# Performance work log

Measured on AMD Instinct MI355X. Metric: run time of the kernel, lower is better.

## Reference

```python
import jax, jax.numpy as jnp
import numpy as np

N = 50000      # nodes
E = 800000     # directed edges (before self-loops)
IN = 128       # input feature dim
HID = 64       # per-head hidden channels (concat=False -> head mean)
H = 4          # attention heads
OUT = 1
NEG_SLOPE = 0.2


def setup_inputs() -> dict:
    key = jax.random.key(0)
    ks = jax.random.split(key, 20)
    def glorot(k, shape, fan):
        return jax.random.normal(k, shape, jnp.float32) * (1.0 / np.sqrt(fan))
    inp = {
        "x": jax.random.normal(ks[0], (N, IN), jnp.float32),
        "edge_index": jax.random.randint(ks[1], (2, E), 0, N, jnp.int32),
        # layer 1
        "W1": glorot(ks[2], (IN, H * HID), IN),
        "a_s1": glorot(ks[3], (H, HID), HID),
        "a_d1": glorot(ks[4], (H, HID), HID),
        "b1": jnp.zeros((HID,), jnp.float32),
        # layer 2
        "W2": glorot(ks[5], (HID, H * HID), HID),
        "a_s2": glorot(ks[6], (H, HID), HID),
        "a_d2": glorot(ks[7], (H, HID), HID),
        "b2": jnp.zeros((HID,), jnp.float32),
        # layer 3
        "W3": glorot(ks[8], (HID, H * HID), HID),
        "a_s3": glorot(ks[9], (H, HID), HID),
        "a_d3": glorot(ks[10], (H, HID), HID),
        "b3": jnp.zeros((HID,), jnp.float32),
        # final linear
        "fc_W": glorot(ks[11], (HID, OUT), HID),
        "fc_b": jnp.zeros((OUT,), jnp.float32),
    }
    return inp


def _gat_layer(x, src, dst, W, a_s, a_d, b):
    """PyG GATConv with concat=False (mean over heads), self-loops already in src/dst."""
    n = x.shape[0]
    h = (x @ W).reshape(n, H, -1)                      # [N,H,C]
    es = jnp.einsum('nhc,hc->nh', h, a_s)              # [N,H] alpha_src per node
    ed = jnp.einsum('nhc,hc->nh', h, a_d)              # [N,H] alpha_dst per node
    e = jax.nn.leaky_relu(es[src] + ed[dst], NEG_SLOPE)  # [E,H] per-edge logits
    # segment softmax over edges sharing the same dst (every node has a self-loop)
    m = jax.ops.segment_max(e, dst, num_segments=n)
    w = jnp.exp(e - m[dst])
    z = jax.ops.segment_sum(w, dst, num_segments=n)
    alpha = w / z[dst]                                  # [E,H]
    out = jax.ops.segment_sum(alpha[:, :, None] * h[src], dst, num_segments=n)  # [N,H,C]
    return out.mean(axis=1) + b                         # concat=False -> head mean + bias


def reference(x, edge_index, W1, a_s1, a_d1, b1, W2, a_s2, a_d2, b2,
              W3, a_s3, a_d3, b3, fc_W, fc_b):
    n = x.shape[0]
    loops = jnp.arange(n, dtype=edge_index.dtype)
    src = jnp.concatenate([edge_index[0], loops])
    dst = jnp.concatenate([edge_index[1], loops])
    gelu = lambda t: jax.nn.gelu(t, approximate=False)  # torch F.gelu default = exact erf
    x = gelu(_gat_layer(x, src, dst, W1, a_s1, a_d1, b1))
    x = gelu(_gat_layer(x, src, dst, W2, a_s2, a_d2, b2))
    x = gelu(_gat_layer(x, src, dst, W3, a_s3, a_d3, b3))
    # dropout is identity in eval mode (deterministic reference)
    return jax.nn.sigmoid(x @ fc_W + fc_b)              # [N,1]
```

## Files before the change

kernel.cpp:

```cpp
#include <hip/hip_runtime.h>
#include <math.h>

#define N_NODES 50000
#define N_EDGES 800000
#define ETOT    (N_EDGES + N_NODES)
#define DIM_IN  128
#define HID     64
#define NHEAD   4
#define HDIM    256
#define NEG_SLOPE 0.2f

typedef __attribute__((ext_vector_type(8))) short bf16x8;
typedef __attribute__((ext_vector_type(4))) float f32x4;

static __device__ __forceinline__ float gelu_exact(float x) {
    return 0.5f * x * (1.0f + erff(x * 0.70710678118654752f));
}
static __device__ __forceinline__ unsigned short f2bf(float f) {
    unsigned u = __float_as_uint(f);
    u = (u + 0x7FFFu + ((u >> 16) & 1u)) >> 16;
    return (unsigned short)u;
}

__global__ void count_conv_kernel(const int* __restrict__ ei, int* __restrict__ counts,
                                  int* __restrict__ eslot,
                                  const float* __restrict__ W1, const float* __restrict__ W2,
                                  const float* __restrict__ W3,
                                  unsigned short* __restrict__ Wt1, unsigned short* __restrict__ Wt2,
                                  unsigned short* __restrict__ Wt3) {
    int i = blockIdx.x * 256 + threadIdx.x;
    if (i < 65536) {
        if (i < 32768) {
            int k = i >> 8, n = i & 255;
            Wt1[n * DIM_IN + k] = f2bf(W1[i]);
        } else if (i < 49152) {
            int l = i - 32768; int k = l >> 8, n = l & 255;
            Wt2[n * HID + k] = f2bf(W2[l]);
        } else {
            int l = i - 49152; int k = l >> 8, n = l & 255;
            Wt3[n * HID + k] = f2bf(W3[l]);
        }
    }
    if (i >= ETOT) return;
    int d = (i < N_EDGES) ? ei[N_EDGES + i] : (i - N_EDGES);
    eslot[i] = atomicAdd(&counts[d], 1);
}

__global__ void scan1_kernel(const int* __restrict__ counts, int* __restrict__ offs,
                             int* __restrict__ blockSums) {
    __shared__ int s[256];
    int t = threadIdx.x, idx = blockIdx.x * 256 + t;
    int v = (idx < N_NODES) ? counts[idx] : 0;
    s[t] = v; __syncthreads();
    #pragma unroll
    for (int o = 1; o < 256; o <<= 1) {
        int add = (t >= o) ? s[t - o] : 0;
        __syncthreads();
        s[t] += add;
        __syncthreads();
    }
    if (idx < N_NODES) offs[idx] = s[t] - v;
    if (t == 255) blockSums[blockIdx.x] = s[t];
}

__global__ void scan2_kernel(const int* __restrict__ blockSums, int* __restrict__ blockScan, int nb) {
    __shared__ int s[256];
    int t = threadIdx.x;
    int v = (t < nb) ? blockSums[t] : 0;
    s[t] = v; __syncthreads();
    #pragma unroll
    for (int o = 1; o < 256; o <<= 1) {
        int add = (t >= o) ? s[t - o] : 0;
        __syncthreads();
        s[t] += add;
        __syncthreads();
    }
    blockScan[t] = s[t] - v;
}

__global__ void scan3_kernel(int* __restrict__ offs, const int* __restrict__ blockScan) {
    int idx = blockIdx.x * 256 + threadIdx.x;
    if (idx < N_NODES) offs[idx] += blockScan[blockIdx.x];
    if (idx == 0) offs[N_NODES] = ETOT;
}

__global__ void fill_kernel(const int* __restrict__ ei, const int* __restrict__ offs,
                            const int* __restrict__ eslot, int* __restrict__ coff) {
    int i = blockIdx.x * 256 + threadIdx.x;
    if (i >= ETOT) return;
    int s, d;
    if (i < N_EDGES) { s = ei[i]; d = ei[N_EDGES + i]; } else { s = d = i - N_EDGES; }
    coff[offs[d] + eslot[i]] = s << 9;
}

template<int K, bool F32A>
__global__ __launch_bounds__(256) void gemm_mfma_kernel(
    const void* __restrict__ Aptr, const unsigned short* __restrict__ Wt,
    const float* __restrict__ a_s, const float* __restrict__ a_d,
    unsigned short* __restrict__ h_bf, float* __restrict__ es, float* __restrict__ ed,
    int M)
{
    constexpr int KS = K / 32;
    __shared__ unsigned short hstage[64][HDIM + 8];
    const int lane = threadIdx.x & 63;
    const int head = threadIdx.x >> 6;
    const int l15 = lane & 15;
    const int lg  = lane >> 4;
    const int row0 = blockIdx.x * 64;

    bf16x8 bfrag[4][KS];
    #pragma unroll
    for (int n = 0; n < 4; ++n)
        #pragma unroll
        for (int ks = 0; ks < KS; ++ks)
            bfrag[n][ks] = *(const bf16x8*)(Wt + (size_t)(head * 64 + n * 16 + l15) * K + ks * 32 + lg * 8);

    f32x4 acc[4][4];
    #pragma unroll
    for (int m = 0; m < 4; ++m)
        #pragma unroll
        for (int n = 0; n < 4; ++n)
            acc[m][n] = (f32x4){0.f, 0.f, 0.f, 0.f};

    #pragma unroll
    for (int m = 0; m < 4; ++m) {
        int row = row0 + m * 16 + l15;
        if (row >= M) row = M - 1;
        #pragma unroll
        for (int ks = 0; ks < KS; ++ks) {
            bf16x8 af;
            if constexpr (F32A) {
                const float* ap = (const float*)Aptr + (size_t)row * K + ks * 32 + lg * 8;
                float4 u0 = *(const float4*)(ap);
                float4 u1 = *(const float4*)(ap + 4);
                af[0] = (short)f2bf(u0.x); af[1] = (short)f2bf(u0.y);
                af[2] = (short)f2bf(u0.z); af[3] = (short)f2bf(u0.w);
                af[4] = (short)f2bf(u1.x); af[5] = (short)f2bf(u1.y);
                af[6] = (short)f2bf(u1.z); af[7] = (short)f2bf(u1.w);
            } else {
                af = *(const bf16x8*)((const unsigned short*)Aptr + (size_t)row * K + ks * 32 + lg * 8);
            }
            #pragma unroll
            for (int n = 0; n < 4; ++n)
                acc[m][n] = __builtin_amdgcn_mfma_f32_16x16x32_bf16(af, bfrag[n][ks], acc[m][n], 0, 0, 0);
        }
    }

    float asv[4], adv[4];
    #pragma unroll
    for (int n = 0; n < 4; ++n) {
        asv[n] = a_s[head * 64 + n * 16 + l15];
        adv[n] = a_d[head * 64 + n * 16 + l15];
    }
    #pragma unroll
    for (int m = 0; m < 4; ++m) {
        #pragma unroll
        for (int r = 0; r < 4; ++r) {
            int rloc = m * 16 + lg * 4 + r;
            float ps = 0.f, pd = 0.f;
            #pragma unroll
            for (int n = 0; n < 4; ++n) {
                float v = acc[m][n][r];
                ps += v * asv[n];
                pd += v * adv[n];
                hstage[rloc][head * 64 + n * 16 + l15] = f2bf(v);
            }
            #pragma unroll
            for (int o = 8; o; o >>= 1) { ps += __shfl_xor(ps, o, 64); pd += __shfl_xor(pd, o, 64); }
            int rg = row0 + rloc;
            if (l15 == 0 && rg < M) { es[rg * 4 + head] = ps; ed[rg * 4 + head] = pd; }
        }
    }
    __syncthreads();
    #pragma unroll
    for (int it = 0; it < 8; ++it) {
        int id = threadIdx.x + it * 256;
        int row = id >> 5, c8 = (id & 31) * 8;
        int rg = row0 + row;
        if (rg < M) {
            int4 v = *(const int4*)(&hstage[row][c8]);
            *(int4*)(h_bf + (size_t)rg * HDIM + c8) = v;
        }
    }
}

static __device__ __forceinline__ float4 lrelu4(float4 e) {
    e.x = (e.x > 0.f) ? e.x : NEG_SLOPE * e.x;
    e.y = (e.y > 0.f) ? e.y : NEG_SLOPE * e.y;
    e.z = (e.z > 0.f) ? e.z : NEG_SLOPE * e.z;
    e.w = (e.w > 0.f) ? e.w : NEG_SLOPE * e.w;
    return e;
}

template<bool LAST>
__global__ __launch_bounds__(256) void gather_kernel(
    const unsigned short* __restrict__ h_bf,
    const float4* __restrict__ es4, const float4* __restrict__ ed4,
    const int* __restrict__ offs, const int* __restrict__ coff,
    const float* __restrict__ bias,
    const float* __restrict__ fcW, const float* __restrict__ fcb,
    unsigned short* __restrict__ xout_bf, float* __restrict__ out)
{
    __shared__ float wls[4][4][72];
    __shared__ int   sls[4][64];
    const int wv   = threadIdx.x >> 6;
    const int lane = threadIdx.x & 63;
    const int w    = blockIdx.x * 4 + wv;
    const int l32  = lane & 31;
    const int half = lane >> 5;
    const int hd8  = l32 >> 3;
    const int beg = offs[w], end = offs[w + 1];
    const int deg = end - beg;
    const float4 edv = ed4[w];
    const char* hch = (const char*)h_bf + l32 * 16;

    float acc[8];
    #pragma unroll
    for (int c = 0; c < 8; ++c) acc[c] = 0.f;
    float4 zac = {0.f, 0.f, 0.f, 0.f};

    if (deg <= 64) {
        float4 e = {-INFINITY, -INFINITY, -INFINITY, -INFINITY};
        int sb = 0;
        if (lane < deg) {
            sb = coff[beg + lane];
            float4 ev = *(const float4*)((const char*)es4 + (((unsigned)sb) >> 5));
            ev.x += edv.x; ev.y += edv.y; ev.z += edv.z; ev.w += edv.w;
            e = lrelu4(ev);
        }
        float4 mx = e;
        #pragma unroll
        for (int o = 32; o; o >>= 1) {
            mx.x = fmaxf(mx.x, __shfl_xor(mx.x, o, 64));
            mx.y = fmaxf(mx.y, __shfl_xor(mx.y, o, 64));
            mx.z = fmaxf(mx.z, __shfl_xor(mx.z, o, 64));
            mx.w = fmaxf(mx.w, __shfl_xor(mx.w, o, 64));
        }
        float4 wt = {0.f, 0.f, 0.f, 0.f};
        if (lane < deg) {
            wt.x = __expf(e.x - mx.x); wt.y = __expf(e.y - mx.y);
            wt.z = __expf(e.z - mx.z); wt.w = __expf(e.w - mx.w);
        }
        sls[wv][lane] = sb;
        wls[wv][0][lane] = wt.x; wls[wv][1][lane] = wt.y;
        wls[wv][2][lane] = wt.z; wls[wv][3][lane] = wt.w;
        zac = wt;
        for (int j = 0; j < deg; j += 4) {
            int j0 = j + half, j1 = j + 2 + half;
            int o0 = sls[wv][j0], o1 = sls[wv][j1];
            float a0 = wls[wv][hd8][j0], a1 = wls[wv][hd8][j1];
            int4 u0 = *(const int4*)(hch + o0);
            int4 u1 = *(const int4*)(hch + o1);
            acc[0] += a0 * __uint_as_float(((unsigned)u0.x) << 16);
            acc[1] += a0 * __uint_as_float(u0.x & 0xffff0000u);
            acc[2] += a0 * __uint_as_float(((unsigned)u0.y) << 16);
            acc[3] += a0 * __uint_as_float(u0.y & 0xffff0000u);
            acc[4] += a0 * __uint_as_float(((unsigned)u0.z) << 16);
            acc[5] += a0 * __uint_as_float(u0.z & 0xffff0000u);
            acc[6] += a0 * __uint_as_float(((unsigned)u0.w) << 16);
            acc[7] += a0 * __uint_as_float(u0.w & 0xffff0000u);
            acc[0] += a1 * __uint_as_float(((unsigned)u1.x) << 16);
            acc[1] += a1 * __uint_as_float(u1.x & 0xffff0000u);
            acc[2] += a1 * __uint_as_float(((unsigned)u1.y) << 16);
            acc[3] += a1 * __uint_as_float(u1.y & 0xffff0000u);
            acc[4] += a1 * __uint_as_float(((unsigned)u1.z) << 16);
            acc[5] += a1 * __uint_as_float(u1.z & 0xffff0000u);
            acc[6] += a1 * __uint_as_float(((unsigned)u1.w) << 16);
            acc[7] += a1 * __uint_as_float(u1.w & 0xffff0000u);
        }
    } else {
        float4 mx = {-INFINITY, -INFINITY, -INFINITY, -INFINITY};
        for (int i = beg + lane; i < end; i += 64) {
            int sb = coff[i];
            float4 ev = *(const float4*)((const char*)es4 + (((unsigned)sb) >> 5));
            ev.x += edv.x; ev.y += edv.y; ev.z += edv.z; ev.w += edv.w;
            ev = lrelu4(ev);
            mx.x = fmaxf(mx.x, ev.x); mx.y = fmaxf(mx.y, ev.y);
            mx.z = fmaxf(mx.z, ev.z); mx.w = fmaxf(mx.w, ev.w);
        }
        #pragma unroll
        for (int o = 32; o; o >>= 1) {
            mx.x = fmaxf(mx.x, __shfl_xor(mx.x, o, 64));
            mx.y = fmaxf(mx.y, __shfl_xor(mx.y, o, 64));
            mx.z = fmaxf(mx.z, __shfl_xor(mx.z, o, 64));
            mx.w = fmaxf(mx.w, __shfl_xor(mx.w, o, 64));
        }
        for (int c0 = beg; c0 < end; c0 += 64) {
            int i = c0 + lane;
            float4 wt = {0.f, 0.f, 0.f, 0.f};
            int sb = 0;
            if (i < end) {
                sb = coff[i];
                float4 ev = *(const float4*)((const char*)es4 + (((unsigned)sb) >> 5));
                ev.x += edv.x; ev.y += edv.y; ev.z += edv.z; ev.w += edv.w;
                ev = lrelu4(ev);
                wt.x = __expf(ev.x - mx.x); wt.y = __expf(ev.y - mx.y);
                wt.z = __expf(ev.z - mx.z); wt.w = __expf(ev.w - mx.w);
            }
            sls[wv][lane] = sb;
            wls[wv][0][lane] = wt.x; wls[wv][1][lane] = wt.y;
            wls[wv][2][lane] = wt.z; wls[wv][3][lane] = wt.w;
            zac.x += wt.x; zac.y += wt.y; zac.z += wt.z; zac.w += wt.w;
            int nb = end - c0; if (nb > 64) nb = 64;
            for (int j = 0; j < nb; j += 4) {
                int j0 = j + half, j1 = j + 2 + half;
                int o0 = sls[wv][j0], o1 = sls[wv][j1];
                float a0 = wls[wv][hd8][j0], a1 = wls[wv][hd8][j1];
                int4 u0 = *(const int4*)(hch + o0);
                int4 u1 = *(const int4*)(hch + o1);
                acc[0] += a0 * __uint_as_float(((unsigned)u0.x) << 16);
                acc[1] += a0 * __uint_as_float(u0.x & 0xffff0000u);
                acc[2] += a0 * __uint_as_float(((unsigned)u0.y) << 16);
                acc[3] += a0 * __uint_as_float(u0.y & 0xffff0000u);
                acc[4] += a0 * __uint_as_float(((unsigned)u0.z) << 16);
                acc[5] += a0 * __uint_as_float(u0.z & 0xffff0000u);
                acc[6] += a0 * __uint_as_float(((unsigned)u0.w) << 16);
                acc[7] += a0 * __uint_as_float(u0.w & 0xffff0000u);
                acc[0] += a1 * __uint_as_float(((unsigned)u1.x) << 16);
                acc[1] += a1 * __uint_as_float(u1.x & 0xffff0000u);
                acc[2] += a1 * __uint_as_float(((unsigned)u1.y) << 16);
                acc[3] += a1 * __uint_as_float(u1.y & 0xffff0000u);
                acc[4] += a1 * __uint_as_float(((unsigned)u1.z) << 16);
                acc[5] += a1 * __uint_as_float(u1.z & 0xffff0000u);
                acc[6] += a1 * __uint_as_float(((unsigned)u1.w) << 16);
                acc[7] += a1 * __uint_as_float(u1.w & 0xffff0000u);
            }
        }
    }

    #pragma unroll
    for (int c = 0; c < 8; ++c) acc[c] += __shfl_xor(acc[c], 32, 64);
    #pragma unroll
    for (int o = 32; o; o >>= 1) {
        zac.x += __shfl_xor(zac.x, o, 64);
        zac.y += __shfl_xor(zac.y, o, 64);
        zac.z += __shfl_xor(zac.z, o, 64);
        zac.w += __shfl_xor(zac.w, o, 64);
    }
    float zz = (hd8 == 0) ? zac.x : (hd8 == 1) ? zac.y : (hd8 == 2) ? zac.z : zac.w;
    float inv = 1.f / zz;
    #pragma unroll
    for (int c = 0; c < 8; ++c) acc[c] *= inv;
    #pragma unroll
    for (int c = 0; c < 8; ++c) {
        acc[c] += __shfl_xor(acc[c], 8, 64);
        acc[c] += __shfl_xor(acc[c], 16, 64);
    }
    const int d0 = (l32 & 7) * 8;
    float4 b0 = *(const float4*)(bias + d0);
    float4 b1 = *(const float4*)(bias + d0 + 4);
    float r[8];
    r[0] = gelu_exact(0.25f * acc[0] + b0.x);
    r[1] = gelu_exact(0.25f * acc[1] + b0.y);
    r[2] = gelu_exact(0.25f * acc[2] + b0.z);
    r[3] = gelu_exact(0.25f * acc[3] + b0.w);
    r[4] = gelu_exact(0.25f * acc[4] + b1.x);
    r[5] = gelu_exact(0.25f * acc[5] + b1.y);
    r[6] = gelu_exact(0.25f * acc[6] + b1.z);
    r[7] = gelu_exact(0.25f * acc[7] + b1.w);
    if (!LAST) {
        if (lane < 8) {
            int4 o4;
            o4.x = (int)((((unsigned)f2bf(r[1])) << 16) | f2bf(r[0]));
            o4.y = (int)((((unsigned)f2bf(r[3])) << 16) | f2bf(r[2]));
            o4.z = (int)((((unsigned)f2bf(r[5])) << 16) | f2bf(r[4]));
            o4.w = (int)((((unsigned)f2bf(r[7])) << 16) | f2bf(r[6]));
            *(int4*)(xout_bf + w * HID + d0) = o4;
        }
    } else {
        float4 f0 = *(const float4*)(fcW + d0);
        float4 f1 = *(const float4*)(fcW + d0 + 4);
        float p = r[0]*f0.x + r[1]*f0.y + r[2]*f0.z + r[3]*f0.w
                + r[4]*f1.x + r[5]*f1.y + r[6]*f1.z + r[7]*f1.w;
        p += __shfl_xor(p, 1, 64);
        p += __shfl_xor(p, 2, 64);
        p += __shfl_xor(p, 4, 64);
        if (lane == 0) out[w] = 1.f / (1.f + __expf(-(p + fcb[0])));
    }
}

extern "C" void kernel_launch(void* const* d_in, const int* in_sizes, int n_in,
                              void* d_out, int out_size, void* d_ws, size_t ws_size,
                              hipStream_t stream) {
    const float* x    = (const float*)d_in[0];
    const int*   ei   = (const int*)d_in[1];
    const float* W1   = (const float*)d_in[2];
    const float* as1  = (const float*)d_in[3];
    const float* ad1  = (const float*)d_in[4];
    const float* b1   = (const float*)d_in[5];
    const float* W2   = (const float*)d_in[6];
    const float* as2  = (const float*)d_in[7];
    const float* ad2  = (const float*)d_in[8];
    const float* b2   = (const float*)d_in[9];
    const float* W3   = (const float*)d_in[10];
    const float* as3  = (const float*)d_in[11];
    const float* ad3  = (const float*)d_in[12];
    const float* b3   = (const float*)d_in[13];
    const float* fcW  = (const float*)d_in[14];
    const float* fcb  = (const float*)d_in[15];
    float* out = (float*)d_out;

    char* ws = (char*)d_ws;
    size_t off = 0;
    auto alloc = [&](size_t bytes) -> void* {
        void* p = ws + off;
        off += (bytes + 255) & ~(size_t)255;
        return p;
    };
    unsigned short* h_bf  = (unsigned short*)alloc((size_t)N_NODES * HDIM * 2);
    unsigned short* xA_bf = (unsigned short*)alloc((size_t)N_NODES * HID * 2);
    unsigned short* xB_bf = (unsigned short*)alloc((size_t)N_NODES * HID * 2);
    unsigned short* Wt1   = (unsigned short*)alloc((size_t)HDIM * DIM_IN * 2);
    unsigned short* Wt2   = (unsigned short*)alloc((size_t)HDIM * HID * 2);
    unsigned short* Wt3   = (unsigned short*)alloc((size_t)HDIM * HID * 2);
    float* esb   = (float*)alloc((size_t)N_NODES * 4 * 4);
    float* edb   = (float*)alloc((size_t)N_NODES * 4 * 4);
    int* offs    = (int*)alloc((size_t)(N_NODES + 1) * 4);
    int* counts  = (int*)alloc((size_t)N_NODES * 4);
    int* bsums   = (int*)alloc(256 * 4);
    int* bscan   = (int*)alloc(256 * 4);
    int* eslot   = (int*)alloc((size_t)ETOT * 4);
    int* coff    = (int*)alloc((size_t)ETOT * 4);

    const int NB  = (N_NODES + 255) / 256;
    const int EB  = (ETOT + 255) / 256;
    const int GB  = (N_NODES + 63) / 64;
    const int AGB = N_NODES / 4;

    hipMemsetAsync(counts, 0, (size_t)N_NODES * 4, stream);
    count_conv_kernel<<<EB, 256, 0, stream>>>(ei, counts, eslot, W1, W2, W3, Wt1, Wt2, Wt3);
    scan1_kernel<<<NB, 256, 0, stream>>>(counts, offs, bsums);
    scan2_kernel<<<1, 256, 0, stream>>>(bsums, bscan, NB);
    scan3_kernel<<<NB, 256, 0, stream>>>(offs, bscan);
    fill_kernel<<<EB, 256, 0, stream>>>(ei, offs, eslot, coff);

    gemm_mfma_kernel<DIM_IN, true><<<GB, 256, 0, stream>>>(x, Wt1, as1, ad1, h_bf, esb, edb, N_NODES);
    gather_kernel<false><<<AGB, 256, 0, stream>>>(h_bf, (const float4*)esb, (const float4*)edb,
                                                  offs, coff, b1, fcW, fcb, xA_bf, out);
    gemm_mfma_kernel<HID, false><<<GB, 256, 0, stream>>>(xA_bf, Wt2, as2, ad2, h_bf, esb, edb, N_NODES);
    gather_kernel<false><<<AGB, 256, 0, stream>>>(h_bf, (const float4*)esb, (const float4*)edb,
                                                  offs, coff, b2, fcW, fcb, xB_bf, out);
    gemm_mfma_kernel<HID, false><<<GB, 256, 0, stream>>>(xB_bf, Wt3, as3, ad3, h_bf, esb, edb, N_NODES);
    gather_kernel<true><<<AGB, 256, 0, stream>>>(h_bf, (const float4*)esb, (const float4*)edb,
                                                 offs, coff, b3, fcW, fcb, xA_bf, out);
}
```

Measured before the change: 425.4 us.

## Assign half-wavefront per node, drop softmax max pass, use tanh-form GELU

```diff
diff --git a/kernel.cpp b/kernel.cpp
--- a/kernel.cpp
+++ b/kernel.cpp
@@ -13,13 +13,14 @@
 typedef __attribute__((ext_vector_type(8))) short bf16x8;
 typedef __attribute__((ext_vector_type(4))) float f32x4;
 
-static __device__ __forceinline__ float gelu_exact(float x) {
-    return 0.5f * x * (1.0f + erff(x * 0.70710678118654752f));
-}
 static __device__ __forceinline__ unsigned short f2bf(float f) {
     unsigned u = __float_as_uint(f);
     u = (u + 0x7FFFu + ((u >> 16) & 1u)) >> 16;
     return (unsigned short)u;
+}
+static __device__ __forceinline__ float gelu_fast(float v) {
+    float t2 = 1.5957691216f * v * fmaf(0.044715f * v, v, 1.0f);
+    return v / (1.0f + __expf(-t2));
 }
 
 __global__ void count_conv_kernel(const int* __restrict__ ei, int* __restrict__ counts,
@@ -191,6 +192,16 @@
     e.w = (e.w > 0.f) ? e.w : NEG_SLOPE * e.w;
     return e;
 }
+static __device__ __forceinline__ void acc8(float* acc, float a, const int4 u) {
+    acc[0] = fmaf(a, __uint_as_float(((unsigned)u.x) << 16), acc[0]);
+    acc[1] = fmaf(a, __uint_as_float(u.x & 0xffff0000u), acc[1]);
+    acc[2] = fmaf(a, __uint_as_float(((unsigned)u.y) << 16), acc[2]);
+    acc[3] = fmaf(a, __uint_as_float(u.y & 0xffff0000u), acc[3]);
+    acc[4] = fmaf(a, __uint_as_float(((unsigned)u.z) << 16), acc[4]);
+    acc[5] = fmaf(a, __uint_as_float(u.z & 0xffff0000u), acc[5]);
+    acc[6] = fmaf(a, __uint_as_float(((unsigned)u.w) << 16), acc[6]);
+    acc[7] = fmaf(a, __uint_as_float(u.w & 0xffff0000u), acc[7]);
+}
 
 template<bool LAST>
 __global__ __launch_bounds__(256) void gather_kernel(
@@ -201,16 +212,15 @@
     const float* __restrict__ fcW, const float* __restrict__ fcb,
     unsigned short* __restrict__ xout_bf, float* __restrict__ out)
 {
-    __shared__ float wls[4][4][72];
-    __shared__ int   sls[4][64];
+    __shared__ float wls[8][4][36];
+    __shared__ int   sls[8][36];
+    const int lane = threadIdx.x & 63;
     const int wv   = threadIdx.x >> 6;
-    const int lane = threadIdx.x & 63;
-    const int w    = blockIdx.x * 4 + wv;
     const int l32  = lane & 31;
-    const int half = lane >> 5;
+    const int gh   = wv * 2 + (lane >> 5);
+    const int w    = blockIdx.x * 8 + gh;
     const int hd8  = l32 >> 3;
-    const int beg = offs[w], end = offs[w + 1];
-    const int deg = end - beg;
+    const int beg  = offs[w], end = offs[w + 1];
     const float4 edv = ed4[w];
     const char* hch = (const char*)h_bf + l32 * 16;
 
@@ -219,163 +229,80 @@
     for (int c = 0; c < 8; ++c) acc[c] = 0.f;
     float4 zac = {0.f, 0.f, 0.f, 0.f};
 
-    if (deg <= 64) {
-        float4 e = {-INFINITY, -INFINITY, -INFINITY, -INFINITY};
+    for (int c0 = beg; c0 < end; c0 += 32) {
+        int nb = end - c0; if (nb > 32) nb = 32;
+        float4 wt = {0.f, 0.f, 0.f, 0.f};
         int sb = 0;
-        if (lane < deg) {
-            sb = coff[beg + lane];
-            float4 ev = *(const float4*)((const char*)es4 + (((unsigned)sb) >> 5));
-            ev.x += edv.x; ev.y += edv.y; ev.z += edv.z; ev.w += edv.w;
-            e = lrelu4(ev);
-        }
-        float4 mx = e;
-        #pragma unroll
-        for (int o = 32; o; o >>= 1) {
-            mx.x = fmaxf(mx.x, __shfl_xor(mx.x, o, 64));
-            mx.y = fmaxf(mx.y, __shfl_xor(mx.y, o, 64));
-            mx.z = fmaxf(mx.z, __shfl_xor(mx.z, o, 64));
-            mx.w = fmaxf(mx.w, __shfl_xor(mx.w, o, 64));
-        }
-        float4 wt = {0.f, 0.f, 0.f, 0.f};
-        if (lane < deg) {
-            wt.x = __expf(e.x - mx.x); wt.y = __expf(e.y - mx.y);
-            wt.z = __expf(e.z - mx.z); wt.w = __expf(e.w - mx.w);
-        }
-        sls[wv][lane] = sb;
-        wls[wv][0][lane] = wt.x; wls[wv][1][lane] = wt.y;
-        wls[wv][2][lane] = wt.z; wls[wv][3][lane] = wt.w;
-        zac = wt;
-        for (int j = 0; j < deg; j += 4) {
-            int j0 = j + half, j1 = j + 2 + half;
-            int o0 = sls[wv][j0], o1 = sls[wv][j1];
-            float a0 = wls[wv][hd8][j0], a1 = wls[wv][hd8][j1];
-            int4 u0 = *(const int4*)(hch + o0);
-            int4 u1 = *(const int4*)(hch + o1);
-            acc[0] += a0 * __uint_as_float(((unsigned)u0.x) << 16);
-            acc[1] += a0 * __uint_as_float(u0.x & 0xffff0000u);
-            acc[2] += a0 * __uint_as_float(((unsigned)u0.y) << 16);
-            acc[3] += a0 * __uint_as_float(u0.y & 0xffff0000u);
-            acc[4] += a0 * __uint_as_float(((unsigned)u0.z) << 16);
-            acc[5] += a0 * __uint_as_float(u0.z & 0xffff0000u);
-            acc[6] += a0 * __uint_as_float(((unsigned)u0.w) << 16);
-            acc[7] += a0 * __uint_as_float(u0.w & 0xffff0000u);
-            acc[0] += a1 * __uint_as_float(((unsigned)u1.x) << 16);
-            acc[1] += a1 * __uint_as_float(u1.x & 0xffff0000u);
-            acc[2] += a1 * __uint_as_float(((unsigned)u1.y) << 16);
-            acc[3] += a1 * __uint_as_float(u1.y & 0xffff0000u);
-            acc[4] += a1 * __uint_as_float(((unsigned)u1.z) << 16);
-            acc[5] += a1 * __uint_as_float(u1.z & 0xffff0000u);
-            acc[6] += a1 * __uint_as_float(((unsigned)u1.w) << 16);
-            acc[7] += a1 * __uint_as_float(u1.w & 0xffff0000u);
-        }
-    } else {
-        float4 mx = {-INFINITY, -INFINITY, -INFINITY, -INFINITY};
-        for (int i = beg + lane; i < end; i += 64) {
-            int sb = coff[i];
+        if (l32 < nb) {
+            sb = coff[c0 + l32];
             float4 ev = *(const float4*)((const char*)es4 + (((unsigned)sb) >> 5));
             ev.x += edv.x; ev.y += edv.y; ev.z += edv.z; ev.w += edv.w;
             ev = lrelu4(ev);
-            mx.x = fmaxf(mx.x, ev.x); mx.y = fmaxf(mx.y, ev.y);
-            mx.z = fmaxf(mx.z, ev.z); mx.w = fmaxf(mx.w, ev.w);
-        }
-        #pragma unroll
-        for (int o = 32; o; o >>= 1) {
-            mx.x = fmaxf(mx.x, __shfl_xor(mx.x, o, 64));
-            mx.y = fmaxf(mx.y, __shfl_xor(mx.y, o, 64));
-            mx.z = fmaxf(mx.z, __shfl_xor(mx.z, o, 64));
-            mx.w = fmaxf(mx.w, __shfl_xor(mx.w, o, 64));
-        }
-        for (int c0 = beg; c0 < end; c0 += 64) {
-            int i = c0 + lane;
-            float4 wt = {0.f, 0.f, 0.f, 0.f};
-            int sb = 0;
-            if (i < end) {
-                sb = coff[i];
-                float4 ev = *(const float4*)((const char*)es4 + (((unsigned)sb) >> 5));
-                ev.x += edv.x; ev.y += edv.y; ev.z += edv.z; ev.w += edv.w;
-                ev = lrelu4(ev);
-                wt.x = __expf(ev.x - mx.x); wt.y = __expf(ev.y - mx.y);
-                wt.z = __expf(ev.z - mx.z); wt.w = __expf(ev.w - mx.w);
-            }
-            sls[wv][lane] = sb;
-            wls[wv][0][lane] = wt.x; wls[wv][1][lane] = wt.y;
-            wls[wv][2][lane] = wt.z; wls[wv][3][lane] = wt.w;
-            zac.x += wt.x; zac.y += wt.y; zac.z += wt.z; zac.w += wt.w;
-            int nb = end - c0; if (nb > 64) nb = 64;
-            for (int j = 0; j < nb; j += 4) {
-                int j0 = j + half, j1 = j + 2 + half;
-                int o0 = sls[wv][j0], o1 = sls[wv][j1];
-                float a0 = wls[wv][hd8][j0], a1 = wls[wv][hd8][j1];
-                int4 u0 = *(const int4*)(hch + o0);
-                int4 u1 = *(const int4*)(hch + o1);
-                acc[0] += a0 * __uint_as_float(((unsigned)u0.x) << 16);
-                acc[1] += a0 * __uint_as_float(u0.x & 0xffff0000u);
-                acc[2] += a0 * __uint_as_float(((unsigned)u0.y) << 16);
-                acc[3] += a0 * __uint_as_float(u0.y & 0xffff0000u);
-                acc[4] += a0 * __uint_as_float(((unsigned)u0.z) << 16);
-                acc[5] += a0 * __uint_as_float(u0.z & 0xffff0000u);
-                acc[6] += a0 * __uint_as_float(((unsigned)u0.w) << 16);
-                acc[7] += a0 * __uint_as_float(u0.w & 0xffff0000u);
-                acc[0] += a1 * __uint_as_float(((unsigned)u1.x) << 16);
-                acc[1] += a1 * __uint_as_float(u1.x & 0xffff0000u);
-                acc[2] += a1 * __uint_as_float(((unsigned)u1.y) << 16);
-                acc[3] += a1 * __uint_as_float(u1.y & 0xffff0000u);
-                acc[4] += a1 * __uint_as_float(((unsigned)u1.z) << 16);
-                acc[5] += a1 * __uint_as_float(u1.z & 0xffff0000u);
-                acc[6] += a1 * __uint_as_float(((unsigned)u1.w) << 16);
-                acc[7] += a1 * __uint_as_float(u1.w & 0xffff0000u);
-            }
-        }
-    }
-
-    #pragma unroll
-    for (int c = 0; c < 8; ++c) acc[c] += __shfl_xor(acc[c], 32, 64);
-    #pragma unroll
-    for (int o = 32; o; o >>= 1) {
-        zac.x += __shfl_xor(zac.x, o, 64);
-        zac.y += __shfl_xor(zac.y, o, 64);
-        zac.z += __shfl_xor(zac.z, o, 64);
-        zac.w += __shfl_xor(zac.w, o, 64);
+            wt.x = __expf(ev.x); wt.y = __expf(ev.y);
+            wt.z = __expf(ev.z); wt.w = __expf(ev.w);
+        }
+        sls[gh][l32] = sb;
+        wls[gh][0][l32] = wt.x; wls[gh][1][l32] = wt.y;
+        wls[gh][2][l32] = wt.z; wls[gh][3][l32] = wt.w;
+        zac.x += wt.x; zac.y += wt.y; zac.z += wt.z; zac.w += wt.w;
+        for (int j = 0; j < nb; j += 4) {
+            int4   s4 = *(const int4*)(&sls[gh][j]);
+            float4 a4 = *(const float4*)(&wls[gh][hd8][j]);
+            int4 u0 = *(const int4*)(hch + s4.x);
+            int4 u1 = *(const int4*)(hch + s4.y);
+            int4 u2 = *(const int4*)(hch + s4.z);
+            int4 u3 = *(const int4*)(hch + s4.w);
+            acc8(acc, a4.x, u0);
+            acc8(acc, a4.y, u1);
+            acc8(acc, a4.z, u2);
+            acc8(acc, a4.w, u3);
+        }
+    }
+
+    #pragma unroll
+    for (int o = 16; o; o >>= 1) {
+        zac.x += __shfl_xor(zac.x, o);
+        zac.y += __shfl_xor(zac.y, o);
+        zac.z += __shfl_xor(zac.z, o);
+        zac.w += __shfl_xor(zac.w, o);
     }
     float zz = (hd8 == 0) ? zac.x : (hd8 == 1) ? zac.y : (hd8 == 2) ? zac.z : zac.w;
     float inv = 1.f / zz;
     #pragma unroll
-    for (int c = 0; c < 8; ++c) acc[c] *= inv;
-    #pragma unroll
     for (int c = 0; c < 8; ++c) {
-        acc[c] += __shfl_xor(acc[c], 8, 64);
-        acc[c] += __shfl_xor(acc[c], 16, 64);
-    }
-    const int d0 = (l32 & 7) * 8;
-    float4 b0 = *(const float4*)(bias + d0);
-    float4 b1 = *(const float4*)(bias + d0 + 4);
-    float r[8];
-    r[0] = gelu_exact(0.25f * acc[0] + b0.x);
-    r[1] = gelu_exact(0.25f * acc[1] + b0.y);
-    r[2] = gelu_exact(0.25f * acc[2] + b0.z);
-    r[3] = gelu_exact(0.25f * acc[3] + b0.w);
-    r[4] = gelu_exact(0.25f * acc[4] + b1.x);
-    r[5] = gelu_exact(0.25f * acc[5] + b1.y);
-    r[6] = gelu_exact(0.25f * acc[6] + b1.z);
-    r[7] = gelu_exact(0.25f * acc[7] + b1.w);
-    if (!LAST) {
-        if (lane < 8) {
+        acc[c] *= inv;
+        acc[c] += __shfl_xor(acc[c], 8);
+        acc[c] += __shfl_xor(acc[c], 16);
+    }
+    if (l32 < 8) {
+        const int d0 = l32 * 8;
+        float4 b0 = *(const float4*)(bias + d0);
+        float4 b1 = *(const float4*)(bias + d0 + 4);
+        float r0 = gelu_fast(0.25f * acc[0] + b0.x);
+        float r1 = gelu_fast(0.25f * acc[1] + b0.y);
+        float r2 = gelu_fast(0.25f * acc[2] + b0.z);
+        float r3 = gelu_fast(0.25f * acc[3] + b0.w);
+        float r4 = gelu_fast(0.25f * acc[4] + b1.x);
+        float r5 = gelu_fast(0.25f * acc[5] + b1.y);
+        float r6 = gelu_fast(0.25f * acc[6] + b1.z);
+        float r7 = gelu_fast(0.25f * acc[7] + b1.w);
+        if (!LAST) {
             int4 o4;
-            o4.x = (int)((((unsigned)f2bf(r[1])) << 16) | f2bf(r[0]));
-            o4.y = (int)((((unsigned)f2bf(r[3])) << 16) | f2bf(r[2]));
-            o4.z = (int)((((unsigned)f2bf(r[5])) << 16) | f2bf(r[4]));
-            o4.w = (int)((((unsigned)f2bf(r[7])) << 16) | f2bf(r[6]));
+            o4.x = (int)((((unsigned)f2bf(r1)) << 16) | f2bf(r0));
+            o4.y = (int)((((unsigned)f2bf(r3)) << 16) | f2bf(r2));
+            o4.z = (int)((((unsigned)f2bf(r5)) << 16) | f2bf(r4));
+            o4.w = (int)((((unsigned)f2bf(r7)) << 16) | f2bf(r6));
             *(int4*)(xout_bf + w * HID + d0) = o4;
-        }
-    } else {
-        float4 f0 = *(const float4*)(fcW + d0);
-        float4 f1 = *(const float4*)(fcW + d0 + 4);
-        float p = r[0]*f0.x + r[1]*f0.y + r[2]*f0.z + r[3]*f0.w
-                + r[4]*f1.x + r[5]*f1.y + r[6]*f1.z + r[7]*f1.w;
-        p += __shfl_xor(p, 1, 64);
-        p += __shfl_xor(p, 2, 64);
-        p += __shfl_xor(p, 4, 64);
-        if (lane == 0) out[w] = 1.f / (1.f + __expf(-(p + fcb[0])));
+        } else {
+            float4 f0 = *(const float4*)(fcW + d0);
+            float4 f1 = *(const float4*)(fcW + d0 + 4);
+            float p = r0*f0.x + r1*f0.y + r2*f0.z + r3*f0.w
+                    + r4*f1.x + r5*f1.y + r6*f1.z + r7*f1.w;
+            p += __shfl_xor(p, 1);
+            p += __shfl_xor(p, 2);
+            p += __shfl_xor(p, 4);
+            if (l32 == 0) out[w] = 1.f / (1.f + __expf(-(p + fcb[0])));
+        }
     }
 }
 
@@ -425,7 +352,7 @@
     const int NB  = (N_NODES + 255) / 256;
     const int EB  = (ETOT + 255) / 256;
     const int GB  = (N_NODES + 63) / 64;
-    const int AGB = N_NODES / 4;
+    const int AGB = N_NODES / 8;
 
     hipMemsetAsync(counts, 0, (size_t)N_NODES * 4, stream);
     count_conv_kernel<<<EB, 256, 0, stream>>>(ei, counts, eslot, W1, W2, W3, Wt1, Wt2, Wt3);
```

After: 408.5 us. 4.0% less time.
